# Kernel optimization log

Hardware: AMD Instinct MI355X
Metric: run time of the kernel (lower is better)

The kernel has to match this reference:

```python
import jax, jax.numpy as jnp
import numpy as np

N_NODES = 100000
N_EDGES = 1600000
IN_C, HID, OUT_C = 100, 128, 47
N_HID_LAYERS = 3  # SAGEConv(hid->hid) count; +1 final SAGEConv(hid->out)


def setup_inputs() -> dict:
    key = jax.random.key(0)
    ks = jax.random.split(key, 8)
    x = jax.random.normal(ks[0], (N_NODES, IN_C), dtype=jnp.float32)
    edge_index = jax.random.randint(ks[1], (2, N_EDGES), 0, N_NODES, dtype=jnp.int32)
    s = 0.05  # weight scale for numeric stability
    return {
        "x": x,
        "edge_index": edge_index,
        "inproj_w": jax.random.normal(ks[2], (IN_C, HID), dtype=jnp.float32) * s,
        "inproj_b": jnp.zeros((HID,), jnp.float32),
        "wl_h": jax.random.normal(ks[3], (N_HID_LAYERS, HID, HID), dtype=jnp.float32) * s,
        "bl_h": jnp.zeros((N_HID_LAYERS, HID), jnp.float32),
        "wr_h": jax.random.normal(ks[4], (N_HID_LAYERS, HID, HID), dtype=jnp.float32) * s,
        "wl_out": jax.random.normal(ks[5], (HID, OUT_C), dtype=jnp.float32) * s,
        "bl_out": jnp.zeros((OUT_C,), jnp.float32),
        "wr_out": jax.random.normal(ks[6], (HID, OUT_C), dtype=jnp.float32) * s,
    }


def reference(x, edge_index, inproj_w, inproj_b, wl_h, bl_h, wr_h, wl_out, bl_out, wr_out):
    n = x.shape[0]
    src, dst = edge_index[0], edge_index[1]
    # in-degree for mean aggregation (clamped to avoid div-by-zero)
    deg = jax.ops.segment_sum(jnp.ones_like(dst, dtype=x.dtype), dst, num_segments=n)
    deg = jnp.maximum(deg, 1.0)[:, None]

    def sage(h, wl, bl, wr):
        # mean over incoming-edge messages, then lin_l(agg) + lin_r(h)
        agg = jax.ops.segment_sum(h[src], dst, num_segments=n) / deg
        return agg @ wl + bl + h @ wr

    h = x @ inproj_w + inproj_b
    inp = h
    h = jax.nn.relu(h)
    for i in range(N_HID_LAYERS):
        h = sage(h, wl_h[i], bl_h[i], wr_h[i])
        h = jax.nn.relu(h) + 0.2 * inp  # dropout is identity in eval mode
    h = sage(h, wl_out, bl_out, wr_out)
    return jax.nn.log_softmax(h, axis=-1)
```

## Files before the change

### kernel.cpp

```cpp
#include <hip/hip_runtime.h>
#include <math.h>

#define HIDC 128
#define INC 100
#define OUTC 47

typedef __attribute__((ext_vector_type(8))) short short8_t;
typedef __attribute__((ext_vector_type(4))) float f32x4;

__device__ inline unsigned short f2bf(float f) {
    unsigned u = __builtin_bit_cast(unsigned, f);
    unsigned r = (u + 0x7FFFu + ((u >> 16) & 1u)) >> 16;
    return (unsigned short)r;
}
__device__ inline float bf2f(unsigned short s) {
    unsigned u = ((unsigned)s) << 16;
    return __builtin_bit_cast(float, u);
}


__global__ __launch_bounds__(256) void k_deg(const int* __restrict__ dst, int* __restrict__ deg, int ne) {
    int e = blockIdx.x * 256 + threadIdx.x;
    if (e < ne) atomicAdd(&deg[dst[e]], 1);
}

__global__ __launch_bounds__(256) void k_scan1(const int* __restrict__ deg, int* __restrict__ local_s,
                                               int* __restrict__ bsum, int n) {
    __shared__ int s[256];
    int t = threadIdx.x;
    int i = blockIdx.x * 256 + t;
    int v = (i < n) ? deg[i] : 0;
    s[t] = v;
    __syncthreads();
    for (int off = 1; off < 256; off <<= 1) {
        int add = (t >= off) ? s[t - off] : 0;
        __syncthreads();
        s[t] += add;
        __syncthreads();
    }
    if (i < n) local_s[i] = s[t] - v;
    if (t == 255) bsum[blockIdx.x] = s[255];
}

__global__ __launch_bounds__(512) void k_scan2(int* __restrict__ bsum, int nb) {
    __shared__ int s[512];
    int t = threadIdx.x;
    int v = (t < nb) ? bsum[t] : 0;
    s[t] = v;
    __syncthreads();
    for (int off = 1; off < 512; off <<= 1) {
        int add = (t >= off) ? s[t - off] : 0;
        __syncthreads();
        s[t] += add;
        __syncthreads();
    }
    if (t < nb) bsum[t] = s[t] - v;
}

__global__ __launch_bounds__(256) void k_scan3(const int* __restrict__ local_s, const int* __restrict__ bsum,
                                               int* __restrict__ offs, int n, int ne) {
    int i = blockIdx.x * 256 + threadIdx.x;
    if (i < n) offs[i] = local_s[i] + bsum[blockIdx.x];
    if (i == 0) offs[n] = ne;
}

__global__ __launch_bounds__(256) void k_invdeg(const int* __restrict__ deg, float* __restrict__ invdeg, int n) {
    int i = blockIdx.x * 256 + threadIdx.x;
    if (i < n) invdeg[i] = 1.0f / (float)max(deg[i], 1);
}


__global__ __launch_bounds__(256) void k_fill(const int* __restrict__ src, const int* __restrict__ dst,
                                              const int* __restrict__ offs, int* __restrict__ curs,
                                              int* __restrict__ csr, int ne, int psize, int ch) {
    int p = blockIdx.x & 7;
    int chunk = blockIdx.x >> 3;
    int lo = p * psize;
    int e0 = chunk * ch;
    int e1 = min(ne, e0 + ch);
    for (int e = e0 + threadIdx.x; e < e1; e += 256) {
        int d = dst[e];
        if ((unsigned)(d - lo) < (unsigned)psize) {
            int pos = atomicAdd(&curs[d], 1);
            csr[offs[d] + pos] = src[e];
        }
    }
}


__global__ __launch_bounds__(256) void k_prepw(const float* __restrict__ wl_h, const float* __restrict__ wr_h,
                                               unsigned short* __restrict__ wt) {
    int idx = blockIdx.x * 256 + threadIdx.x;
    if (idx >= 6 * 16384) return;
    int m = idx >> 14, rem = idx & 16383;
    int l = m >> 1, s = m & 1;
    const float* srcm = (s == 0 ? wl_h : wr_h) + (size_t)l * 16384;
    wt[idx] = f2bf(srcm[(rem & 127) * 128 + (rem >> 7)]);
}

__global__ __launch_bounds__(256) void k_prepw_out(const float* __restrict__ wl_out,
                                                   const float* __restrict__ wr_out,
                                                   unsigned short* __restrict__ wt2) {
    int idx = blockIdx.x * 256 + threadIdx.x;
    if (idx >= 2 * 48 * 128) return;
    int s = idx / (48 * 128), rem = idx % (48 * 128);
    int nc = rem >> 7, k = rem & 127;
    const float* srcm = (s == 0) ? wl_out : wr_out;
    wt2[idx] = (nc < OUTC) ? f2bf(srcm[k * OUTC + nc]) : 0;
}


__global__ __launch_bounds__(256) void k_agg(const unsigned short* __restrict__ h, const int* __restrict__ csr,
                                             const int* __restrict__ offs, const float* __restrict__ invdeg,
                                             unsigned short* __restrict__ agg, int n) {
    int wv = threadIdx.x >> 6, lane = threadIdx.x & 63;
    int v = blockIdx.x * 4 + wv;
    if (v >= n) return;
    int q = lane >> 4, c = lane & 15;
    int e0 = offs[v], e1 = offs[v + 1];
    float acc[8] = {0, 0, 0, 0, 0, 0, 0, 0};
    for (int e = e0 + q; e < e1; e += 8) {
        int s0 = csr[e];
        bool has2 = (e + 4) < e1;
        int s1 = has2 ? csr[e + 4] : s0;
        short8_t t0 = *reinterpret_cast<const short8_t*>(h + (size_t)s0 * HIDC + c * 8);
        short8_t t1 = *reinterpret_cast<const short8_t*>(h + (size_t)s1 * HIDC + c * 8);
#pragma unroll
        for (int i = 0; i < 8; i++) {
            acc[i] += bf2f((unsigned short)t0[i]);
            if (has2) acc[i] += bf2f((unsigned short)t1[i]);
        }
    }
#pragma unroll
    for (int i = 0; i < 8; i++) {
        acc[i] += __shfl_xor(acc[i], 16);
        acc[i] += __shfl_xor(acc[i], 32);
    }
    if (q == 0) {
        float s = invdeg[v];
        unsigned short o[8];
#pragma unroll
        for (int i = 0; i < 8; i++) o[i] = f2bf(acc[i] * s);
        *reinterpret_cast<short8_t*>(agg + (size_t)v * HIDC + c * 8) = *reinterpret_cast<const short8_t*>(o);
    }
}


__global__ __launch_bounds__(256) void k_inproj(const float* __restrict__ x, const float* __restrict__ w,
                                                const float* __restrict__ b, float* __restrict__ inp,
                                                unsigned short* __restrict__ h, int n) {
    __shared__ float sX[16][INC];
    int t = threadIdx.x;
    int brow = blockIdx.x * 16;
    for (int idx = t; idx < 16 * INC; idx += 256) {
        int r = idx / INC, c = idx % INC;
        int row = brow + r;
        sX[r][c] = (row < n) ? x[(size_t)row * INC + c] : 0.f;
    }
    __syncthreads();
    int q = t >> 6, j = t & 63;
    float acc0[4] = {0, 0, 0, 0}, acc1[4] = {0, 0, 0, 0};
#pragma unroll 2
    for (int k0 = 0; k0 < INC; k0 += 4) {
        float a_[4][4];
#pragma unroll
        for (int r = 0; r < 4; r++) {
            float4 t4 = *reinterpret_cast<const float4*>(&sX[q * 4 + r][k0]);
            a_[r][0] = t4.x; a_[r][1] = t4.y; a_[r][2] = t4.z; a_[r][3] = t4.w;
        }
#pragma unroll
        for (int kk = 0; kk < 4; kk++) {
            int k = k0 + kk;
            float w0 = w[k * HIDC + j];
            float w1 = w[k * HIDC + j + 64];
#pragma unroll
            for (int r = 0; r < 4; r++) {
                acc0[r] += a_[r][kk] * w0;
                acc1[r] += a_[r][kk] * w1;
            }
        }
    }
    float b0 = b[j], b1 = b[j + 64];
#pragma unroll
    for (int r = 0; r < 4; r++) {
        int row = brow + q * 4 + r;
        if (row < n) {
            float v0 = acc0[r] + b0, v1 = acc1[r] + b1;
            inp[(size_t)row * HIDC + j] = v0;
            inp[(size_t)row * HIDC + j + 64] = v1;
            h[(size_t)row * HIDC + j] = f2bf(fmaxf(v0, 0.f));
            h[(size_t)row * HIDC + j + 64] = f2bf(fmaxf(v1, 0.f));
        }
    }
}


__global__ __launch_bounds__(256) void k_sage_mfma(const unsigned short* __restrict__ agg,
                                                   unsigned short* __restrict__ h,
                                                   const float* __restrict__ inp,
                                                   const unsigned short* __restrict__ wt,
                                                   const float* __restrict__ bl, int n) {
    __shared__ unsigned short sA[2][32 * 128];
    int t = threadIdx.x;
    int w = t >> 6, lane = t & 63;
    int cc = lane & 15, kg = lane >> 4;
    int row0 = blockIdx.x * 32;

    short8_t bfrag[2][2][4];
#pragma unroll
    for (int s = 0; s < 2; s++)
#pragma unroll
        for (int ci = 0; ci < 2; ci++) {
            int ncol = 32 * w + ci * 16 + cc;
            const unsigned short* bp = wt + s * 16384 + ncol * 128 + kg * 8;
#pragma unroll
            for (int ks = 0; ks < 4; ks++)
                bfrag[s][ci][ks] = *reinterpret_cast<const short8_t*>(bp + ks * 32);
        }

    for (int c = t; c < 512; c += 256) {
        int r = c >> 4, g = c & 15;
        int row = row0 + r;
        unsigned byte = r * 256 + (((unsigned)g * 16) ^ (((unsigned)r & 7) << 4));
        short8_t va = {0, 0, 0, 0, 0, 0, 0, 0}, vh = va;
        if (row < n) {
            va = *reinterpret_cast<const short8_t*>(agg + (size_t)row * HIDC + g * 8);
            vh = *reinterpret_cast<const short8_t*>(h + (size_t)row * HIDC + g * 8);
        }
        *reinterpret_cast<short8_t*>(reinterpret_cast<char*>(&sA[0][0]) + byte) = va;
        *reinterpret_cast<short8_t*>(reinterpret_cast<char*>(&sA[1][0]) + byte) = vh;
    }
    __syncthreads();

    f32x4 acc[2][2];
#pragma unroll
    for (int rt = 0; rt < 2; rt++)
#pragma unroll
        for (int ci = 0; ci < 2; ci++) acc[rt][ci] = (f32x4){0.f, 0.f, 0.f, 0.f};

#pragma unroll
    for (int ks = 0; ks < 4; ks++) {
        short8_t af[2][2];
#pragma unroll
        for (int s = 0; s < 2; s++)
#pragma unroll
            for (int rt = 0; rt < 2; rt++) {
                int r = rt * 16 + cc;
                unsigned byte = r * 256 + (((unsigned)(ks * 64 + kg * 16)) ^ (((unsigned)r & 7) << 4));
                af[s][rt] = *reinterpret_cast<const short8_t*>(reinterpret_cast<const char*>(&sA[s][0]) + byte);
            }
#pragma unroll
        for (int s = 0; s < 2; s++)
#pragma unroll
            for (int rt = 0; rt < 2; rt++)
#pragma unroll
                for (int ci = 0; ci < 2; ci++)
                    acc[rt][ci] = __builtin_amdgcn_mfma_f32_16x16x32_bf16(af[s][rt], bfrag[s][ci][ks],
                                                                          acc[rt][ci], 0, 0, 0);
    }

#pragma unroll
    for (int rt = 0; rt < 2; rt++)
#pragma unroll
        for (int ci = 0; ci < 2; ci++) {
            int col = 32 * w + ci * 16 + cc;
            float bv = bl[col];
#pragma unroll
            for (int reg = 0; reg < 4; reg++) {
                int row = row0 + rt * 16 + kg * 4 + reg;
                if (row < n) {
                    float v = acc[rt][ci][reg] + bv;
                    v = fmaxf(v, 0.f) + 0.2f * inp[(size_t)row * HIDC + col];
                    h[(size_t)row * HIDC + col] = f2bf(v);
                }
            }
        }
}


__global__ __launch_bounds__(256) void k_out_mfma(const unsigned short* __restrict__ agg,
                                                  const unsigned short* __restrict__ h,
                                                  const unsigned short* __restrict__ wt2,
                                                  const float* __restrict__ bl,
                                                  float* __restrict__ out, int n) {
    __shared__ unsigned short sA[2][64 * 128];
    int t = threadIdx.x;
    int w = t >> 6, lane = t & 63;
    int cc = lane & 15, kg = lane >> 4;
    int row0 = blockIdx.x * 64;

    short8_t bfrag[2][3][4];
#pragma unroll
    for (int s = 0; s < 2; s++)
#pragma unroll
        for (int ci = 0; ci < 3; ci++) {
            const unsigned short* bp = wt2 + s * (48 * 128) + (ci * 16 + cc) * 128 + kg * 8;
#pragma unroll
            for (int ks = 0; ks < 4; ks++)
                bfrag[s][ci][ks] = *reinterpret_cast<const short8_t*>(bp + ks * 32);
        }

    for (int c = t; c < 1024; c += 256) {
        int r = c >> 4, g = c & 15;
        int row = row0 + r;
        unsigned byte = r * 256 + (((unsigned)g * 16) ^ (((unsigned)r & 7) << 4));
        short8_t va = {0, 0, 0, 0, 0, 0, 0, 0}, vh = va;
        if (row < n) {
            va = *reinterpret_cast<const short8_t*>(agg + (size_t)row * HIDC + g * 8);
            vh = *reinterpret_cast<const short8_t*>(h + (size_t)row * HIDC + g * 8);
        }
        *reinterpret_cast<short8_t*>(reinterpret_cast<char*>(&sA[0][0]) + byte) = va;
        *reinterpret_cast<short8_t*>(reinterpret_cast<char*>(&sA[1][0]) + byte) = vh;
    }
    __syncthreads();

    f32x4 acc[3];
#pragma unroll
    for (int ci = 0; ci < 3; ci++) acc[ci] = (f32x4){0.f, 0.f, 0.f, 0.f};

#pragma unroll
    for (int ks = 0; ks < 4; ks++) {
        short8_t af[2];
        int r = w * 16 + cc;
        unsigned byte = r * 256 + (((unsigned)(ks * 64 + kg * 16)) ^ (((unsigned)r & 7) << 4));
#pragma unroll
        for (int s = 0; s < 2; s++)
            af[s] = *reinterpret_cast<const short8_t*>(reinterpret_cast<const char*>(&sA[s][0]) + byte);
#pragma unroll
        for (int s = 0; s < 2; s++)
#pragma unroll
            for (int ci = 0; ci < 3; ci++)
                acc[ci] = __builtin_amdgcn_mfma_f32_16x16x32_bf16(af[s], bfrag[s][ci][ks], acc[ci], 0, 0, 0);
    }

#pragma unroll
    for (int reg = 0; reg < 4; reg++) {
        int row = row0 + w * 16 + kg * 4 + reg;
        float val[3];
        float m = -INFINITY;
#pragma unroll
        for (int ci = 0; ci < 3; ci++) {
            int col = ci * 16 + cc;
            val[ci] = (col < OUTC) ? (acc[ci][reg] + bl[col]) : -INFINITY;
            m = fmaxf(m, val[ci]);
        }
#pragma unroll
        for (int off = 1; off < 16; off <<= 1) m = fmaxf(m, __shfl_xor(m, off));
        float s = 0.f;
#pragma unroll
        for (int ci = 0; ci < 3; ci++) {
            int col = ci * 16 + cc;
            if (col < OUTC) s += __expf(val[ci] - m);
        }
#pragma unroll
        for (int off = 1; off < 16; off <<= 1) s += __shfl_xor(s, off);
        float lse = m + logf(s);
        if (row < n) {
#pragma unroll
            for (int ci = 0; ci < 3; ci++) {
                int col = ci * 16 + cc;
                if (col < OUTC) out[(size_t)row * OUTC + col] = val[ci] - lse;
            }
        }
    }
}


extern "C" void kernel_launch(void* const* d_in, const int* in_sizes, int n_in,
                              void* d_out, int out_size, void* d_ws, size_t ws_size,
                              hipStream_t stream) {
    const float* x        = (const float*)d_in[0];
    const int*   ei       = (const int*)d_in[1];
    const float* inproj_w = (const float*)d_in[2];
    const float* inproj_b = (const float*)d_in[3];
    const float* wl_h     = (const float*)d_in[4];
    const float* bl_h     = (const float*)d_in[5];
    const float* wr_h     = (const float*)d_in[6];
    const float* wl_out   = (const float*)d_in[7];
    const float* bl_out   = (const float*)d_in[8];
    const float* wr_out   = (const float*)d_in[9];
    float* out = (float*)d_out;

    int n  = in_sizes[0] / INC;
    int ne = in_sizes[1] / 2;
    const int* src = ei;
    const int* dst = ei + ne;

    char* ws = (char*)d_ws;
    size_t off = 0;
    auto alloc = [&](size_t bytes) -> void* {
        void* p = ws + off;
        off = (off + bytes + 255) & ~(size_t)255;
        return p;
    };
    float*          inp    = (float*)alloc((size_t)n * HIDC * 4);
    unsigned short* h      = (unsigned short*)alloc((size_t)n * HIDC * 2);
    unsigned short* agg    = (unsigned short*)alloc((size_t)n * HIDC * 2);
    unsigned short* wt     = (unsigned short*)alloc((size_t)6 * 16384 * 2);
    unsigned short* wt2    = (unsigned short*)alloc((size_t)2 * 48 * 128 * 2);
    int*   deg    = (int*)alloc((size_t)n * 4);
    float* invdeg = (float*)alloc((size_t)n * 4);
    int*   local_s= (int*)alloc((size_t)n * 4);
    int*   bsum   = (int*)alloc(512 * 4);
    int*   offs   = (int*)alloc((size_t)(n + 1) * 4);
    int*   curs   = (int*)alloc((size_t)n * 4);
    int*   csr    = (int*)alloc((size_t)ne * 4);

    hipMemsetAsync(deg, 0, (size_t)n * 4, stream);
    hipMemsetAsync(curs, 0, (size_t)n * 4, stream);

    int nbE = (ne + 255) / 256;
    int nbN = (n + 255) / 256;
    k_deg<<<nbE, 256, 0, stream>>>(dst, deg, ne);
    k_scan1<<<nbN, 256, 0, stream>>>(deg, local_s, bsum, n);
    k_scan2<<<1, 512, 0, stream>>>(bsum, nbN);
    k_scan3<<<nbN, 256, 0, stream>>>(local_s, bsum, offs, n, ne);
    k_invdeg<<<nbN, 256, 0, stream>>>(deg, invdeg, n);

    int psize = (n + 7) / 8;
    int nchunk = 256;
    int ch = (ne + nchunk - 1) / nchunk;
    k_fill<<<nchunk * 8, 256, 0, stream>>>(src, dst, offs, curs, csr, ne, psize, ch);

    k_prepw<<<(6 * 16384 + 255) / 256, 256, 0, stream>>>(wl_h, wr_h, wt);
    k_prepw_out<<<(2 * 48 * 128 + 255) / 256, 256, 0, stream>>>(wl_out, wr_out, wt2);

    int nbR = (n + 15) / 16;
    int nbA = (n + 3) / 4;
    int nbT = (n + 31) / 32;
    int nbO = (n + 63) / 64;
    k_inproj<<<nbR, 256, 0, stream>>>(x, inproj_w, inproj_b, inp, h, n);
    for (int l = 0; l < 3; ++l) {
        k_agg<<<nbA, 256, 0, stream>>>(h, csr, offs, invdeg, agg, n);
        k_sage_mfma<<<nbT, 256, 0, stream>>>(agg, h, inp, wt + (size_t)l * 2 * 16384,
                                             bl_h + (size_t)l * HIDC, n);
    }
    k_agg<<<nbA, 256, 0, stream>>>(h, csr, offs, invdeg, agg, n);
    k_out_mfma<<<nbO, 256, 0, stream>>>(agg, h, wt2, bl_out, out, n);
}
```

Measured before the change: 631.7 us.

## Move input projection to bf16 MFMA and store residual input as bf16

Replaces the scalar fp32 FMA input projection with a bf16 MFMA kernel that uses pre-transposed, zero-padded weights and a swizzled LDS tile of x converted to bf16. The residual tensor inp is also stored as bf16, halving its write traffic and its reads in each of the three hidden SAGE layers. In exchange, the input projection and the residual term lose precision to bf16 rounding, and an extra small weight-prep launch is added.

Measured after the change: 592.3 us. -6.2%, faster.

```diff
diff --git a/kernel.cpp b/kernel.cpp
--- a/kernel.cpp
+++ b/kernel.cpp
@@ -107,6 +107,14 @@
     int nc = rem >> 7, k = rem & 127;
     const float* srcm = (s == 0) ? wl_out : wr_out;
     wt2[idx] = (nc < OUTC) ? f2bf(srcm[k * OUTC + nc]) : 0;
+}
+
+__global__ __launch_bounds__(256) void k_prepw_in(const float* __restrict__ w,
+                                                  unsigned short* __restrict__ wtin) {
+    int idx = blockIdx.x * 256 + threadIdx.x;
+    if (idx >= 128 * 128) return;
+    int nc = idx >> 7, k = idx & 127;
+    wtin[idx] = (k < INC) ? f2bf(w[k * HIDC + nc]) : 0;
 }
 
 
@@ -146,58 +154,104 @@
 }
 
 
-__global__ __launch_bounds__(256) void k_inproj(const float* __restrict__ x, const float* __restrict__ w,
-                                                const float* __restrict__ b, float* __restrict__ inp,
-                                                unsigned short* __restrict__ h, int n) {
-    __shared__ float sX[16][INC];
+__global__ __launch_bounds__(256) void k_inproj_mfma(const float* __restrict__ x,
+                                                     const unsigned short* __restrict__ wtin,
+                                                     const float* __restrict__ b,
+                                                     unsigned short* __restrict__ inp,
+                                                     unsigned short* __restrict__ h, int n) {
+    __shared__ unsigned short sX[32 * 128];
     int t = threadIdx.x;
-    int brow = blockIdx.x * 16;
-    for (int idx = t; idx < 16 * INC; idx += 256) {
-        int r = idx / INC, c = idx % INC;
-        int row = brow + r;
-        sX[r][c] = (row < n) ? x[(size_t)row * INC + c] : 0.f;
+    int w = t >> 6, lane = t & 63;
+    int cc = lane & 15, kg = lane >> 4;
+    int row0 = blockIdx.x * 32;
+
+    short8_t bfrag[2][4];
+#pragma unroll
+    for (int ci = 0; ci < 2; ci++) {
+        int ncol = 32 * w + ci * 16 + cc;
+        const unsigned short* bp = wtin + ncol * 128 + kg * 8;
+#pragma unroll
+        for (int ks = 0; ks < 4; ks++)
+            bfrag[ci][ks] = *reinterpret_cast<const short8_t*>(bp + ks * 32);
+    }
+
+    {
+        int r = t >> 3, seg = t & 7;
+        int row = row0 + r;
+        float v[16];
+#pragma unroll
+        for (int i = 0; i < 16; i++) v[i] = 0.f;
+        if (row < n) {
+            const float* xr = x + (size_t)row * INC;
+            if (seg < 6) {
+#pragma unroll
+                for (int j = 0; j < 4; j++) {
+                    float4 f = *reinterpret_cast<const float4*>(xr + seg * 16 + j * 4);
+                    v[j * 4 + 0] = f.x; v[j * 4 + 1] = f.y; v[j * 4 + 2] = f.z; v[j * 4 + 3] = f.w;
+                }
+            } else if (seg == 6) {
+                float4 f = *reinterpret_cast<const float4*>(xr + 96);
+                v[0] = f.x; v[1] = f.y; v[2] = f.z; v[3] = f.w;
+            }
+        }
+        unsigned short o[16];
+#pragma unroll
+        for (int i = 0; i < 16; i++) o[i] = f2bf(v[i]);
+#pragma unroll
+        for (int half = 0; half < 2; half++) {
+            int g = seg * 2 + half;
+            unsigned byte = r * 256 + (((unsigned)g * 16) ^ (((unsigned)r & 7) << 4));
+            *reinterpret_cast<short8_t*>(reinterpret_cast<char*>(sX) + byte) =
+                *reinterpret_cast<const short8_t*>(&o[half * 8]);
+        }
     }
     __syncthreads();
-    int q = t >> 6, j = t & 63;
-    float acc0[4] = {0, 0, 0, 0}, acc1[4] = {0, 0, 0, 0};
-#pragma unroll 2
-    for (int k0 = 0; k0 < INC; k0 += 4) {
-        float a_[4][4];
-#pragma unroll
-        for (int r = 0; r < 4; r++) {
-            float4 t4 = *reinterpret_cast<const float4*>(&sX[q * 4 + r][k0]);
-            a_[r][0] = t4.x; a_[r][1] = t4.y; a_[r][2] = t4.z; a_[r][3] = t4.w;
-        }
-#pragma unroll
-        for (int kk = 0; kk < 4; kk++) {
-            int k = k0 + kk;
-            float w0 = w[k * HIDC + j];
-            float w1 = w[k * HIDC + j + 64];
-#pragma unroll
-            for (int r = 0; r < 4; r++) {
-                acc0[r] += a_[r][kk] * w0;
-                acc1[r] += a_[r][kk] * w1;
+
+    f32x4 acc[2][2];
+#pragma unroll
+    for (int rt = 0; rt < 2; rt++)
+#pragma unroll
+        for (int ci = 0; ci < 2; ci++) acc[rt][ci] = (f32x4){0.f, 0.f, 0.f, 0.f};
+
+#pragma unroll
+    for (int ks = 0; ks < 4; ks++) {
+        short8_t af[2];
+#pragma unroll
+        for (int rt = 0; rt < 2; rt++) {
+            int r = rt * 16 + cc;
+            unsigned byte = r * 256 + (((unsigned)(ks * 64 + kg * 16)) ^ (((unsigned)r & 7) << 4));
+            af[rt] = *reinterpret_cast<const short8_t*>(reinterpret_cast<const char*>(sX) + byte);
+        }
+#pragma unroll
+        for (int rt = 0; rt < 2; rt++)
+#pragma unroll
+            for (int ci = 0; ci < 2; ci++)
+                acc[rt][ci] = __builtin_amdgcn_mfma_f32_16x16x32_bf16(af[rt], bfrag[ci][ks],
+                                                                      acc[rt][ci], 0, 0, 0);
+    }
+
+#pragma unroll
+    for (int rt = 0; rt < 2; rt++)
+#pragma unroll
+        for (int ci = 0; ci < 2; ci++) {
+            int col = 32 * w + ci * 16 + cc;
+            float bv = b[col];
+#pragma unroll
+            for (int reg = 0; reg < 4; reg++) {
+                int row = row0 + rt * 16 + kg * 4 + reg;
+                if (row < n) {
+                    float v = acc[rt][ci][reg] + bv;
+                    inp[(size_t)row * HIDC + col] = f2bf(v);
+                    h[(size_t)row * HIDC + col] = f2bf(fmaxf(v, 0.f));
+                }
             }
         }
-    }
-    float b0 = b[j], b1 = b[j + 64];
-#pragma unroll
-    for (int r = 0; r < 4; r++) {
-        int row = brow + q * 4 + r;
-        if (row < n) {
-            float v0 = acc0[r] + b0, v1 = acc1[r] + b1;
-            inp[(size_t)row * HIDC + j] = v0;
-            inp[(size_t)row * HIDC + j + 64] = v1;
-            h[(size_t)row * HIDC + j] = f2bf(fmaxf(v0, 0.f));
-            h[(size_t)row * HIDC + j + 64] = f2bf(fmaxf(v1, 0.f));
-        }
-    }
 }
 
 
 __global__ __launch_bounds__(256) void k_sage_mfma(const unsigned short* __restrict__ agg,
                                                    unsigned short* __restrict__ h,
-                                                   const float* __restrict__ inp,
+                                                   const unsigned short* __restrict__ inp,
                                                    const unsigned short* __restrict__ wt,
                                                    const float* __restrict__ bl, int n) {
     __shared__ unsigned short sA[2][32 * 128];
@@ -270,7 +324,7 @@
                 int row = row0 + rt * 16 + kg * 4 + reg;
                 if (row < n) {
                     float v = acc[rt][ci][reg] + bv;
-                    v = fmaxf(v, 0.f) + 0.2f * inp[(size_t)row * HIDC + col];
+                    v = fmaxf(v, 0.f) + 0.2f * bf2f(inp[(size_t)row * HIDC + col]);
                     h[(size_t)row * HIDC + col] = f2bf(v);
                 }
             }
@@ -393,11 +447,12 @@
         off = (off + bytes + 255) & ~(size_t)255;
         return p;
     };
-    float*          inp    = (float*)alloc((size_t)n * HIDC * 4);
+    unsigned short* inp    = (unsigned short*)alloc((size_t)n * HIDC * 2);
     unsigned short* h      = (unsigned short*)alloc((size_t)n * HIDC * 2);
     unsigned short* agg    = (unsigned short*)alloc((size_t)n * HIDC * 2);
     unsigned short* wt     = (unsigned short*)alloc((size_t)6 * 16384 * 2);
     unsigned short* wt2    = (unsigned short*)alloc((size_t)2 * 48 * 128 * 2);
+    unsigned short* wtin   = (unsigned short*)alloc((size_t)128 * 128 * 2);
     int*   deg    = (int*)alloc((size_t)n * 4);
     float* invdeg = (float*)alloc((size_t)n * 4);
     int*   local_s= (int*)alloc((size_t)n * 4);
@@ -424,12 +479,12 @@
 
     k_prepw<<<(6 * 16384 + 255) / 256, 256, 0, stream>>>(wl_h, wr_h, wt);
     k_prepw_out<<<(2 * 48 * 128 + 255) / 256, 256, 0, stream>>>(wl_out, wr_out, wt2);
-
-    int nbR = (n + 15) / 16;
+    k_prepw_in<<<(128 * 128 + 255) / 256, 256, 0, stream>>>(inproj_w, wtin);
+
     int nbA = (n + 3) / 4;
     int nbT = (n + 31) / 32;
     int nbO = (n + 63) / 64;
-    k_inproj<<<nbR, 256, 0, stream>>>(x, inproj_w, inproj_b, inp, h, n);
+    k_inproj_mfma<<<nbT, 256, 0, stream>>>(x, wtin, inproj_b, inp, h, n);
     for (int l = 0; l < 3; ++l) {
         k_agg<<<nbA, 256, 0, stream>>>(h, csr, offs, invdeg, agg, n);
         k_sage_mfma<<<nbT, 256, 0, stream>>>(agg, h, inp, wt + (size_t)l * 2 * 16384,
```
